# Kernel optimization log

Measured on AMD Instinct MI355X. Metric: run time of the kernel, lower is better.

Reference implementation:

```python
import jax, jax.numpy as jnp
import numpy as np
from jax.scipy.special import logsumexp

NUM_CANONICAL = 558
NUM_ITERS = 5
TEMPERATURE = 1.0


def setup_inputs() -> dict:
    key = jax.random.key(0)
    k1, k2 = jax.random.split(key)
    B, N, C = 32, 4096, NUM_CANONICAL
    scores = jax.random.normal(k1, (B, N, C), dtype=jnp.float32)
    visible_mask = jax.random.randint(k2, (B, N), 0, 2).astype(bool)
    dustbin_col_score = jnp.asarray(-1.0, dtype=jnp.float32)  # learned scalar param
    return {"scores": scores, "visible_mask": visible_mask,
            "dustbin_col_score": dustbin_col_score}


def _log_sinkhorn(aug_scores, log_mu, log_nu, iters):
    # aug_scores: [B,N,M], log_mu: [B,N], log_nu: [B,M]
    B, N, M = aug_scores.shape
    log_u = jnp.zeros((B, N), dtype=aug_scores.dtype)
    log_v = jnp.zeros((B, M), dtype=aug_scores.dtype)
    for _ in range(iters):
        log_u = log_mu - logsumexp(aug_scores + log_v[:, None, :], axis=-1)
        log_v = log_nu - logsumexp(aug_scores + log_u[:, :, None], axis=1)
    return jnp.exp(aug_scores + log_u[:, :, None] + log_v[:, None, :])


def reference(scores, visible_mask, dustbin_col_score):
    B, N, C = scores.shape
    scaled = scores / TEMPERATURE
    dust = jnp.broadcast_to(dustbin_col_score / TEMPERATURE, (B, N, 1))
    aug = jnp.concatenate([scaled, dust], axis=-1)  # [B, N, C+1]

    # source marginals: uniform over visible nodes, -inf (mass 0) otherwise
    num_vis = jnp.sum(visible_mask, axis=1).astype(aug.dtype)  # [B]
    log_mu = jnp.where(visible_mask, -jnp.log(num_vis)[:, None], -jnp.inf)
    # target marginals: uniform over C canonical ids + dustbin column
    log_nu = jnp.full((B, C + 1), jnp.log(1.0 / (C + 1)), dtype=aug.dtype)

    full_assignments = _log_sinkhorn(aug, log_mu, log_nu, NUM_ITERS)  # [B,N,C+1]
    soft_assignments = full_assignments[:, :, :-1]
    hard_assignments = jnp.argmax(soft_assignments, axis=-1)
    dustbin_weights = full_assignments[:, :, -1:]
    return full_assignments, soft_assignments, hard_assignments, dustbin_weights
```

## Files before the change

### kernel.cpp

```cpp
#include <hip/hip_runtime.h>
#include <cstddef>


namespace {
constexpr int B_ = 32, N_ = 4096, C_ = 558, M_ = 559, MP_ = 560;

constexpr size_t U_OFF = 0;
constexpr size_t V_OFF = (size_t)B_ * N_;
constexpr size_t A_OFF = V_OFF + (size_t)B_ * MP_;
constexpr size_t I_OFF = A_OFF + (size_t)B_ * MP_;

constexpr size_t FULL_OFF = 0;
constexpr size_t SOFT_OFF = (size_t)B_ * N_ * M_;
constexpr size_t HARD_OFF = SOFT_OFF + (size_t)B_ * N_ * C_;
constexpr size_t DUST_OFF = HARD_OFF + (size_t)B_ * N_;
}

__global__ void k_init(const int* __restrict__ vm, float* __restrict__ ws) {
    const int b = blockIdx.x;
    const int tid = threadIdx.x;
    __shared__ int red[256];
    int s = 0;
    for (int n = tid; n < N_; n += 256) s += (vm[(size_t)b * N_ + n] != 0);
    red[tid] = s;
    __syncthreads();
    for (int off = 128; off > 0; off >>= 1) {
        if (tid < off) red[tid] += red[tid + off];
        __syncthreads();
    }
    if (tid == 0) ws[I_OFF + b] = 1.0f / (float)red[0];
    for (int c = tid; c < MP_; c += 256) {
        ws[V_OFF + (size_t)b * MP_ + c] = 1.0f;
        ws[A_OFF + (size_t)b * MP_ + c] = 0.0f;
    }
}

__global__ __launch_bounds__(256) void k_row(const float* __restrict__ sc,
                                             const int* __restrict__ vm,
                                             const float* __restrict__ dustp,
                                             float* __restrict__ ws) {
    const int b = blockIdx.y;
    const int chunk = blockIdx.x;
    const int wave = threadIdx.x >> 6;
    const int lane = threadIdx.x & 63;

    const float dustE = expf(dustp[0]);
    const float invnv = ws[I_OFF + b];
    const float* __restrict__ vrow = ws + V_OFF + (size_t)b * MP_;
    float* __restrict__ acc = ws + A_OFF + (size_t)b * MP_;

    float2 v2[4];
#pragma unroll
    for (int k = 0; k < 4; ++k)
        v2[k] = *(const float2*)(vrow + k * 128 + 2 * lane);
    float vt = 0.0f;
    if (lane < 46) vt = vrow[512 + lane];
    else if (lane == 46) vt = vrow[558];

    float2 a2[4] = {{0.f, 0.f}, {0.f, 0.f}, {0.f, 0.f}, {0.f, 0.f}};
    float at = 0.0f;

    const int row0 = chunk * 128 + wave * 32;
    for (int r = 0; r < 32; ++r) {
        const int n = row0 + r;
        const float* __restrict__ srow = sc + (size_t)(b * N_ + n) * C_;

        float2 e2[4];
#pragma unroll
        for (int k = 0; k < 4; ++k) {
            float2 x = *(const float2*)(srow + k * 128 + 2 * lane);
            e2[k].x = expf(x.x);
            e2[k].y = expf(x.y);
        }
        float et = 0.0f;
        if (lane < 46) et = expf(srow[512 + lane]);
        else if (lane == 46) et = dustE;

        float s = et * vt;
#pragma unroll
        for (int k = 0; k < 4; ++k)
            s += e2[k].x * v2[k].x + e2[k].y * v2[k].y;
#pragma unroll
        for (int m = 1; m < 64; m <<= 1) s += __shfl_xor(s, m, 64);

        const int vis = vm[(size_t)b * N_ + n];
        const float u = vis ? (invnv / s) : 0.0f;
        if (lane == 0) ws[U_OFF + (size_t)b * N_ + n] = u;

#pragma unroll
        for (int k = 0; k < 4; ++k) {
            a2[k].x += e2[k].x * u;
            a2[k].y += e2[k].y * u;
        }
        at += et * u;
    }

#pragma unroll
    for (int k = 0; k < 4; ++k) {
        atomicAdd(&acc[k * 128 + 2 * lane], a2[k].x);
        atomicAdd(&acc[k * 128 + 2 * lane + 1], a2[k].y);
    }
    if (lane <= 46) atomicAdd(&acc[512 + lane], at);
}

__global__ void k_vupd(float* __restrict__ ws) {
    const int b = blockIdx.x;
    const float nu = 1.0f / 559.0f;
    for (int c = threadIdx.x; c < M_; c += 256) {
        const float a = ws[A_OFF + (size_t)b * MP_ + c];
        ws[V_OFF + (size_t)b * MP_ + c] = nu / a;
        ws[A_OFF + (size_t)b * MP_ + c] = 0.0f;
    }
}

__global__ __launch_bounds__(256) void k_final(const float* __restrict__ sc,
                                               const float* __restrict__ dustp,
                                               const float* __restrict__ ws,
                                               float* __restrict__ out) {
    const int b = blockIdx.y;
    const int chunk = blockIdx.x;
    const int wave = threadIdx.x >> 6;
    const int lane = threadIdx.x & 63;

    const float dustE = expf(dustp[0]);
    const float* __restrict__ vrow = ws + V_OFF + (size_t)b * MP_;

    float2 v2[4];
#pragma unroll
    for (int k = 0; k < 4; ++k)
        v2[k] = *(const float2*)(vrow + k * 128 + 2 * lane);
    float vt = 0.0f;
    if (lane < 46) vt = vrow[512 + lane];
    else if (lane == 46) vt = vrow[558];

    const int row0 = chunk * 128 + wave * 32;
    for (int r = 0; r < 32; ++r) {
        const int n = row0 + r;
        const float* __restrict__ srow = sc + (size_t)(b * N_ + n) * C_;
        const float u = ws[U_OFF + (size_t)b * N_ + n];

        float2 e2[4];
#pragma unroll
        for (int k = 0; k < 4; ++k) {
            float2 x = *(const float2*)(srow + k * 128 + 2 * lane);
            e2[k].x = expf(x.x);
            e2[k].y = expf(x.y);
        }
        float et = 0.0f;
        if (lane < 46) et = expf(srow[512 + lane]);
        else if (lane == 46) et = dustE;

        float2 p2[4];
#pragma unroll
        for (int k = 0; k < 4; ++k) {
            p2[k].x = e2[k].x * u * v2[k].x;
            p2[k].y = e2[k].y * u * v2[k].y;
        }
        const float pt = et * u * vt;

        float* __restrict__ fr = out + FULL_OFF + (size_t)(b * N_ + n) * M_;
#pragma unroll
        for (int k = 0; k < 4; ++k) {
            fr[k * 128 + 2 * lane] = p2[k].x;
            fr[k * 128 + 2 * lane + 1] = p2[k].y;
        }
        if (lane <= 46) fr[512 + lane] = pt;

        float* __restrict__ so = out + SOFT_OFF + (size_t)(b * N_ + n) * C_;
#pragma unroll
        for (int k = 0; k < 4; ++k)
            *(float2*)(so + k * 128 + 2 * lane) = p2[k];
        if (lane < 46) so[512 + lane] = pt;

        if (lane == 46) out[DUST_OFF + (size_t)b * N_ + n] = pt;

        float best = -1.0f;
        int bidx = 0x7fffffff;
#pragma unroll
        for (int k = 0; k < 4; ++k) {
            const int c = k * 128 + 2 * lane;
            if (p2[k].x > best) { best = p2[k].x; bidx = c; }
            if (p2[k].y > best) { best = p2[k].y; bidx = c + 1; }
        }
        if (lane < 46 && pt > best) { best = pt; bidx = 512 + lane; }
#pragma unroll
        for (int m = 1; m < 64; m <<= 1) {
            const float ov = __shfl_xor(best, m, 64);
            const int oi = __shfl_xor(bidx, m, 64);
            if (ov > best || (ov == best && oi < bidx)) { best = ov; bidx = oi; }
        }
        if (lane == 0) out[HARD_OFF + (size_t)b * N_ + n] = (float)bidx;
    }
}

extern "C" void kernel_launch(void* const* d_in, const int* in_sizes, int n_in,
                              void* d_out, int out_size, void* d_ws, size_t ws_size,
                              hipStream_t stream) {
    const float* sc = (const float*)d_in[0];
    const int* vm = (const int*)d_in[1];
    const float* dustp = (const float*)d_in[2];
    float* out = (float*)d_out;
    float* ws = (float*)d_ws;

    k_init<<<B_, 256, 0, stream>>>(vm, ws);
    for (int it = 0; it < 5; ++it) {
        k_row<<<dim3(32, B_), 256, 0, stream>>>(sc, vm, dustp, ws);
        k_vupd<<<B_, 256, 0, stream>>>(ws);
    }
    k_final<<<dim3(32, B_), 256, 0, stream>>>(sc, dustp, ws, out);
}
```

Before: 1.188 ms.

## Compact visible rows, skip invisible score reads, prefetch next row, nontemporal stores

```diff
diff --git a/kernel.cpp b/kernel.cpp
--- a/kernel.cpp
+++ b/kernel.cpp
@@ -9,50 +9,83 @@
 constexpr size_t V_OFF = (size_t)B_ * N_;
 constexpr size_t A_OFF = V_OFF + (size_t)B_ * MP_;
 constexpr size_t I_OFF = A_OFF + (size_t)B_ * MP_;
+constexpr size_t NV_OFF = I_OFF + B_;
+constexpr size_t VIS_OFF = NV_OFF + B_;
 
 constexpr size_t FULL_OFF = 0;
 constexpr size_t SOFT_OFF = (size_t)B_ * N_ * M_;
 constexpr size_t HARD_OFF = SOFT_OFF + (size_t)B_ * N_ * C_;
 constexpr size_t DUST_OFF = HARD_OFF + (size_t)B_ * N_;
+
+typedef float f2_t __attribute__((ext_vector_type(2)));
+
+__device__ __forceinline__ void st_nt(float* p, float v) {
+    __builtin_nontemporal_store(v, p);
+}
+__device__ __forceinline__ void st_nt2(float* p, float a, float b) {
+    f2_t v; v.x = a; v.y = b;
+    __builtin_nontemporal_store(v, (f2_t*)p);
+}
 }
 
 __global__ void k_init(const int* __restrict__ vm, float* __restrict__ ws) {
     const int b = blockIdx.x;
-    const int tid = threadIdx.x;
-    __shared__ int red[256];
-    int s = 0;
-    for (int n = tid; n < N_; n += 256) s += (vm[(size_t)b * N_ + n] != 0);
-    red[tid] = s;
+    const int t = threadIdx.x;
+    const int* __restrict__ row = vm + (size_t)b * N_;
+    int* __restrict__ visl = ((int*)ws) + VIS_OFF + (size_t)b * N_;
+
+    int m[16];
+    int cnt = 0;
+#pragma unroll
+    for (int j = 0; j < 16; ++j) { m[j] = (row[j * 256 + t] != 0); cnt += m[j]; }
+
+    __shared__ int scn[256];
+    scn[t] = cnt;
     __syncthreads();
-    for (int off = 128; off > 0; off >>= 1) {
-        if (tid < off) red[tid] += red[tid + off];
+    for (int off = 1; off < 256; off <<= 1) {
+        const int add = (t >= off) ? scn[t - off] : 0;
         __syncthreads();
-    }
-    if (tid == 0) ws[I_OFF + b] = 1.0f / (float)red[0];
-    for (int c = tid; c < MP_; c += 256) {
+        scn[t] += add;
+        __syncthreads();
+    }
+    const int inc = scn[t];
+    const int nv = scn[255];
+    int vp = inc - cnt;
+    int ip = N_ - 1 - (16 * t - vp);
+#pragma unroll
+    for (int j = 0; j < 16; ++j) {
+        const int n = j * 256 + t;
+        if (m[j]) visl[vp++] = n;
+        else      visl[ip--] = n;
+    }
+
+    if (t == 0) {
+        ws[I_OFF + b] = 1.0f / (float)nv;
+        ((int*)ws)[NV_OFF + b] = nv;
+    }
+    for (int c = t; c < MP_; c += 256) {
         ws[V_OFF + (size_t)b * MP_ + c] = 1.0f;
         ws[A_OFF + (size_t)b * MP_ + c] = 0.0f;
     }
 }
 
 __global__ __launch_bounds__(256) void k_row(const float* __restrict__ sc,
-                                             const int* __restrict__ vm,
                                              const float* __restrict__ dustp,
                                              float* __restrict__ ws) {
     const int b = blockIdx.y;
-    const int chunk = blockIdx.x;
-    const int wave = threadIdx.x >> 6;
+    const int wid = blockIdx.x * 4 + (threadIdx.x >> 6);
     const int lane = threadIdx.x & 63;
 
     const float dustE = expf(dustp[0]);
     const float invnv = ws[I_OFF + b];
+    const int nv = ((const int*)ws)[NV_OFF + b];
+    const int* __restrict__ visl = ((const int*)ws) + VIS_OFF + (size_t)b * N_;
     const float* __restrict__ vrow = ws + V_OFF + (size_t)b * MP_;
     float* __restrict__ acc = ws + A_OFF + (size_t)b * MP_;
 
     float2 v2[4];
 #pragma unroll
-    for (int k = 0; k < 4; ++k)
-        v2[k] = *(const float2*)(vrow + k * 128 + 2 * lane);
+    for (int k = 0; k < 4; ++k) v2[k] = *(const float2*)(vrow + k * 128 + 2 * lane);
     float vt = 0.0f;
     if (lane < 46) vt = vrow[512 + lane];
     else if (lane == 46) vt = vrow[558];
@@ -60,39 +93,53 @@
     float2 a2[4] = {{0.f, 0.f}, {0.f, 0.f}, {0.f, 0.f}, {0.f, 0.f}};
     float at = 0.0f;
 
-    const int row0 = chunk * 128 + wave * 32;
-    for (int r = 0; r < 32; ++r) {
-        const int n = row0 + r;
-        const float* __restrict__ srow = sc + (size_t)(b * N_ + n) * C_;
+    int i = wid;
+    int n_cur = (i < nv) ? visl[i] : -1;
+    float2 x[4];
+    float xt = 0.0f;
+    if (n_cur >= 0) {
+        const float* __restrict__ srow = sc + (size_t)(b * N_ + n_cur) * C_;
+#pragma unroll
+        for (int k = 0; k < 4; ++k) x[k] = *(const float2*)(srow + k * 128 + 2 * lane);
+        if (lane < 46) xt = srow[512 + lane];
+    }
+
+    while (n_cur >= 0) {
+        const int n_nxt = (i + 128 < nv) ? visl[i + 128] : -1;
+        float2 y[4];
+        float yt = 0.0f;
+        if (n_nxt >= 0) {
+            const float* __restrict__ srow = sc + (size_t)(b * N_ + n_nxt) * C_;
+#pragma unroll
+            for (int k = 0; k < 4; ++k) y[k] = *(const float2*)(srow + k * 128 + 2 * lane);
+            if (lane < 46) yt = srow[512 + lane];
+        }
 
         float2 e2[4];
 #pragma unroll
-        for (int k = 0; k < 4; ++k) {
-            float2 x = *(const float2*)(srow + k * 128 + 2 * lane);
-            e2[k].x = expf(x.x);
-            e2[k].y = expf(x.y);
-        }
+        for (int k = 0; k < 4; ++k) { e2[k].x = expf(x[k].x); e2[k].y = expf(x[k].y); }
         float et = 0.0f;
-        if (lane < 46) et = expf(srow[512 + lane]);
+        if (lane < 46) et = expf(xt);
         else if (lane == 46) et = dustE;
 
         float s = et * vt;
 #pragma unroll
-        for (int k = 0; k < 4; ++k)
-            s += e2[k].x * v2[k].x + e2[k].y * v2[k].y;
+        for (int k = 0; k < 4; ++k) s += e2[k].x * v2[k].x + e2[k].y * v2[k].y;
 #pragma unroll
         for (int m = 1; m < 64; m <<= 1) s += __shfl_xor(s, m, 64);
 
-        const int vis = vm[(size_t)b * N_ + n];
-        const float u = vis ? (invnv / s) : 0.0f;
-        if (lane == 0) ws[U_OFF + (size_t)b * N_ + n] = u;
-
-#pragma unroll
-        for (int k = 0; k < 4; ++k) {
-            a2[k].x += e2[k].x * u;
-            a2[k].y += e2[k].y * u;
-        }
+        const float u = invnv / s;
+        if (lane == 0) ws[U_OFF + (size_t)b * N_ + n_cur] = u;
+
+#pragma unroll
+        for (int k = 0; k < 4; ++k) { a2[k].x += e2[k].x * u; a2[k].y += e2[k].y * u; }
         at += et * u;
+
+        i += 128;
+        n_cur = n_nxt;
+#pragma unroll
+        for (int k = 0; k < 4; ++k) x[k] = y[k];
+        xt = yt;
     }
 
 #pragma unroll
@@ -118,61 +165,74 @@
                                                const float* __restrict__ ws,
                                                float* __restrict__ out) {
     const int b = blockIdx.y;
-    const int chunk = blockIdx.x;
-    const int wave = threadIdx.x >> 6;
+    const int wid = blockIdx.x * 4 + (threadIdx.x >> 6);
     const int lane = threadIdx.x & 63;
 
     const float dustE = expf(dustp[0]);
+    const int nv = ((const int*)ws)[NV_OFF + b];
+    const int* __restrict__ visl = ((const int*)ws) + VIS_OFF + (size_t)b * N_;
     const float* __restrict__ vrow = ws + V_OFF + (size_t)b * MP_;
 
     float2 v2[4];
 #pragma unroll
-    for (int k = 0; k < 4; ++k)
-        v2[k] = *(const float2*)(vrow + k * 128 + 2 * lane);
+    for (int k = 0; k < 4; ++k) v2[k] = *(const float2*)(vrow + k * 128 + 2 * lane);
     float vt = 0.0f;
     if (lane < 46) vt = vrow[512 + lane];
     else if (lane == 46) vt = vrow[558];
 
-    const int row0 = chunk * 128 + wave * 32;
-    for (int r = 0; r < 32; ++r) {
-        const int n = row0 + r;
-        const float* __restrict__ srow = sc + (size_t)(b * N_ + n) * C_;
-        const float u = ws[U_OFF + (size_t)b * N_ + n];
+    int i = wid;
+    int n_cur = (i < nv) ? visl[i] : -1;
+    float2 x[4];
+    float xt = 0.0f, ucur = 0.0f;
+    if (n_cur >= 0) {
+        const float* __restrict__ srow = sc + (size_t)(b * N_ + n_cur) * C_;
+#pragma unroll
+        for (int k = 0; k < 4; ++k) x[k] = *(const float2*)(srow + k * 128 + 2 * lane);
+        if (lane < 46) xt = srow[512 + lane];
+        ucur = ws[U_OFF + (size_t)b * N_ + n_cur];
+    }
+
+    while (n_cur >= 0) {
+        const int n_nxt = (i + 128 < nv) ? visl[i + 128] : -1;
+        float2 y[4];
+        float yt = 0.0f, unxt = 0.0f;
+        if (n_nxt >= 0) {
+            const float* __restrict__ srow = sc + (size_t)(b * N_ + n_nxt) * C_;
+#pragma unroll
+            for (int k = 0; k < 4; ++k) y[k] = *(const float2*)(srow + k * 128 + 2 * lane);
+            if (lane < 46) yt = srow[512 + lane];
+            unxt = ws[U_OFF + (size_t)b * N_ + n_nxt];
+        }
 
         float2 e2[4];
 #pragma unroll
-        for (int k = 0; k < 4; ++k) {
-            float2 x = *(const float2*)(srow + k * 128 + 2 * lane);
-            e2[k].x = expf(x.x);
-            e2[k].y = expf(x.y);
-        }
+        for (int k = 0; k < 4; ++k) { e2[k].x = expf(x[k].x); e2[k].y = expf(x[k].y); }
         float et = 0.0f;
-        if (lane < 46) et = expf(srow[512 + lane]);
+        if (lane < 46) et = expf(xt);
         else if (lane == 46) et = dustE;
 
         float2 p2[4];
 #pragma unroll
         for (int k = 0; k < 4; ++k) {
-            p2[k].x = e2[k].x * u * v2[k].x;
-            p2[k].y = e2[k].y * u * v2[k].y;
-        }
-        const float pt = et * u * vt;
-
-        float* __restrict__ fr = out + FULL_OFF + (size_t)(b * N_ + n) * M_;
-#pragma unroll
-        for (int k = 0; k < 4; ++k) {
-            fr[k * 128 + 2 * lane] = p2[k].x;
-            fr[k * 128 + 2 * lane + 1] = p2[k].y;
-        }
-        if (lane <= 46) fr[512 + lane] = pt;
-
-        float* __restrict__ so = out + SOFT_OFF + (size_t)(b * N_ + n) * C_;
-#pragma unroll
-        for (int k = 0; k < 4; ++k)
-            *(float2*)(so + k * 128 + 2 * lane) = p2[k];
-        if (lane < 46) so[512 + lane] = pt;
-
-        if (lane == 46) out[DUST_OFF + (size_t)b * N_ + n] = pt;
+            p2[k].x = e2[k].x * ucur * v2[k].x;
+            p2[k].y = e2[k].y * ucur * v2[k].y;
+        }
+        const float pt = et * ucur * vt;
+
+        float* __restrict__ fr = out + FULL_OFF + (size_t)(b * N_ + n_cur) * M_;
+#pragma unroll
+        for (int k = 0; k < 4; ++k) {
+            st_nt(fr + k * 128 + 2 * lane, p2[k].x);
+            st_nt(fr + k * 128 + 2 * lane + 1, p2[k].y);
+        }
+        if (lane <= 46) st_nt(fr + 512 + lane, pt);
+
+        float* __restrict__ so = out + SOFT_OFF + (size_t)(b * N_ + n_cur) * C_;
+#pragma unroll
+        for (int k = 0; k < 4; ++k) st_nt2(so + k * 128 + 2 * lane, p2[k].x, p2[k].y);
+        if (lane < 46) st_nt(so + 512 + lane, pt);
+
+        if (lane == 46) st_nt(out + DUST_OFF + (size_t)b * N_ + n_cur, pt);
 
         float best = -1.0f;
         int bidx = 0x7fffffff;
@@ -189,7 +249,33 @@
             const int oi = __shfl_xor(bidx, m, 64);
             if (ov > best || (ov == best && oi < bidx)) { best = ov; bidx = oi; }
         }
-        if (lane == 0) out[HARD_OFF + (size_t)b * N_ + n] = (float)bidx;
+        if (lane == 0) st_nt(out + HARD_OFF + (size_t)b * N_ + n_cur, (float)bidx);
+
+        i += 128;
+        n_cur = n_nxt;
+#pragma unroll
+        for (int k = 0; k < 4; ++k) x[k] = y[k];
+        xt = yt;
+        ucur = unxt;
+    }
+
+    for (int j = nv + wid; j < N_; j += 128) {
+        const int n = visl[j];
+        float* __restrict__ fr = out + FULL_OFF + (size_t)(b * N_ + n) * M_;
+#pragma unroll
+        for (int k = 0; k < 4; ++k) {
+            st_nt(fr + k * 128 + 2 * lane, 0.0f);
+            st_nt(fr + k * 128 + 2 * lane + 1, 0.0f);
+        }
+        if (lane <= 46) st_nt(fr + 512 + lane, 0.0f);
+
+        float* __restrict__ so = out + SOFT_OFF + (size_t)(b * N_ + n) * C_;
+#pragma unroll
+        for (int k = 0; k < 4; ++k) st_nt2(so + k * 128 + 2 * lane, 0.0f, 0.0f);
+        if (lane < 46) st_nt(so + 512 + lane, 0.0f);
+
+        if (lane == 0) st_nt(out + HARD_OFF + (size_t)b * N_ + n, 0.0f);
+        if (lane == 46) st_nt(out + DUST_OFF + (size_t)b * N_ + n, 0.0f);
     }
 }
 
@@ -204,7 +290,7 @@
 
     k_init<<<B_, 256, 0, stream>>>(vm, ws);
     for (int it = 0; it < 5; ++it) {
-        k_row<<<dim3(32, B_), 256, 0, stream>>>(sc, vm, dustp, ws);
+        k_row<<<dim3(32, B_), 256, 0, stream>>>(sc, dustp, ws);
         k_vupd<<<B_, 256, 0, stream>>>(ws);
     }
     k_final<<<dim3(32, B_), 256, 0, stream>>>(sc, dustp, ws, out);
```

Result: faster. 1.039 ms (-12.6%).
